# Kernel optimization log

Hardware: AMD Instinct MI355X
Metric: run time of the kernel (lower is better)

The kernel has to match this reference:

```python
import jax, jax.numpy as jnp
import numpy as np

L = 262144
C = 64           # in_channels == out_channels (required by zeros_like scatter)
NUM_MODES = 64

def setup_inputs() -> dict:
    key = jax.random.key(0)
    k1, k2, k3, k4 = jax.random.split(key, 4)
    u = jax.random.normal(k1, (L, C), dtype=jnp.float32)
    y = jax.random.uniform(k2, (1, 1), dtype=jnp.float32)
    scale = 1.0 / (C * C)
    K = scale * jax.random.normal(k3, (2, C, C, NUM_MODES), dtype=jnp.float32)
    # glorot_normal for square (C, C)
    W = jax.random.normal(k4, (C, C), dtype=jnp.float32) * jnp.sqrt(2.0 / (C + C))
    return {"u": u, "y": y, "K": K, "W": W}

def reference(u, y, K, W):
    num_modes = K.shape[-1]
    out_ch = W.shape[0]
    # conditioner: spectral (global) branch
    u_hat = jnp.fft.rfft(u, axis=0)                      # (L//2+1, C) complex64
    Kc = K[0] + 1j * K[1]                                # (C, C, num_modes)
    z_modes = jnp.einsum('xi,iox->xo', u_hat[:num_modes], Kc)  # (num_modes, C)
    z_global = jnp.zeros_like(u_hat).at[:num_modes, :].set(z_modes)
    # conditioner: local branch (gather one spatial row, apply W)
    length = u.shape[0]
    idx = jnp.int32(y * length)[0][0]
    z_local = jnp.dot(W, u[idx, :out_ch])                # (C,)
    # basefield: inverse transform + local shift
    n = 2 * (z_global.shape[0] - 1)                      # == L
    s = jnp.fft.irfft(z_global, n=n, axis=0)             # (L, C)
    return s + z_local
```

## Files before the change

### kernel.cpp

```cpp
#include <hip/hip_runtime.h>

#define LN 262144
#define LMASK 262143
#define NCH 64
#define NBF 512
#define INV_L (1.0f/262144.0f)
#define BSTR 38
#define ISTR 138
#define XSTR 66

typedef short short8 __attribute__((ext_vector_type(8)));
typedef float f32x4 __attribute__((ext_vector_type(4)));

union s8i4 { int4 i; short8 s; };

static __device__ __forceinline__ unsigned pkbf(float lo, float hi) {
    union { float f; unsigned u; } a, b; a.f = lo; b.f = hi;
    return __builtin_amdgcn_perm(b.u, a.u, 0x07060302u);
}
static __device__ __forceinline__ short8 pk8(const float* v) {
    s8i4 cv;
    cv.i = make_int4(pkbf(v[0], v[1]), pkbf(v[2], v[3]),
                     pkbf(v[4], v[5]), pkbf(v[6], v[7]));
    return cv.s;
}
static __device__ __forceinline__ unsigned short f2bf_t(float x) {
    union { float f; unsigned u; } v; v.f = x;
    return (unsigned short)(v.u >> 16);
}
static __device__ __forceinline__ float bf2f(unsigned short b) {
    union { unsigned u; float f; } v; v.u = ((unsigned)b) << 16;
    return v.f;
}
static __device__ __forceinline__ float fsin01(float rev) {
    float r; asm("v_sin_f32 %0, %1" : "=v"(r) : "v"(rev)); return r;
}
static __device__ __forceinline__ float fcos01(float rev) {
    float r; asm("v_cos_f32 %0, %1" : "=v"(r) : "v"(rev)); return r;
}

__global__ __launch_bounds__(256, 2) void fno_fwd(const float* __restrict__ u,
                                                  unsigned* __restrict__ part_w) {
    __shared__ __align__(16) unsigned short Bt[4][64 * BSTR];
    const int tid = threadIdx.x;
    const int lane = tid & 63;
    const int w = tid >> 6;
    const int l15 = lane & 15;
    const int hk = lane >> 4;
    const int kkst = tid >> 3;
    const int gst = tid & 7;
    const int n0 = blockIdx.x * 512;
    const int m = w * 16 + l15;

    float cR[8], nsR[8];
    #pragma unroll
    for (int j = 0; j < 8; ++j) {
        int ph = (m * (n0 + hk * 8 + j)) & LMASK;
        cR[j] = fcos01((float)ph * INV_L);
        nsR[j] = -fsin01((float)ph * INV_L);
    }
    float cD, sD;
    {
        int ph = (m * 32) & LMASK;
        cD = fcos01((float)ph * INV_L);
        sD = fsin01((float)ph * INV_L);
    }

    f32x4 accC[4], accS[4];
    #pragma unroll
    for (int t = 0; t < 4; ++t) { accC[t] = (f32x4){0,0,0,0}; accS[t] = (f32x4){0,0,0,0}; }

    const float* __restrict__ ub = u + (size_t)(n0 + kkst) * NCH + gst * 8;
    const size_t sub = 32 * NCH;
    const size_t sup = 64 * NCH;

#define STAGE(BUF, VA, VB) do {                                            \
        float uv_[8] = {(VA).x, (VA).y, (VA).z, (VA).w,                    \
                        (VB).x, (VB).y, (VB).z, (VB).w};                   \
        _Pragma("unroll")                                                  \
        for (int q_ = 0; q_ < 8; ++q_)                                     \
            Bt[BUF][(gst * 8 + q_) * BSTR + kkst] = f2bf_t(uv_[q_]);       \
    } while (0)

    float4 r0a = *(const float4*)(ub);
    float4 r0b = *(const float4*)(ub + 4);
    float4 r1a = *(const float4*)(ub + sub);
    float4 r1b = *(const float4*)(ub + sub + 4);
    STAGE(0, r0a, r0b);
    STAGE(1, r1a, r1b);
    r0a = *(const float4*)(ub + sup);
    r0b = *(const float4*)(ub + sup + 4);
    r1a = *(const float4*)(ub + sup + sub);
    r1b = *(const float4*)(ub + sup + sub + 4);

    for (int ss = 0; ss < 8; ++ss) {
        __syncthreads();
        const int cp = ss & 1;
        if (ss + 1 < 8) {
            STAGE((cp ^ 1) * 2 + 0, r0a, r0b);
            STAGE((cp ^ 1) * 2 + 1, r1a, r1b);
        }
        if (ss + 2 < 8) {
            const float* pn = ub + (size_t)(ss + 2) * sup;
            r0a = *(const float4*)(pn);
            r0b = *(const float4*)(pn + 4);
            r1a = *(const float4*)(pn + sub);
            r1b = *(const float4*)(pn + sub + 4);
        }
        #pragma unroll
        for (int st = 0; st < 2; ++st) {
            const short8 aC = pk8(cR);
            const short8 aS = pk8(nsR);
            #pragma unroll
            for (int j = 0; j < 8; ++j) {
                float c2 = cR[j] * cD + nsR[j] * sD;
                nsR[j] = nsR[j] * cD - cR[j] * sD;
                cR[j] = c2;
            }
            const unsigned short* bt = Bt[cp * 2 + st];
            #pragma unroll
            for (int tn = 0; tn < 4; ++tn) {
                const short8 bf = *(const short8*)&bt[(tn * 16 + l15) * BSTR + hk * 8];
                accC[tn] = __builtin_amdgcn_mfma_f32_16x16x32_bf16(aC, bf, accC[tn], 0, 0, 0);
                accS[tn] = __builtin_amdgcn_mfma_f32_16x16x32_bf16(aS, bf, accS[tn], 0, 0, 0);
            }
        }
    }
#undef STAGE
    unsigned* basew = part_w + (size_t)blockIdx.x * 4096;
    #pragma unroll
    for (int tn = 0; tn < 4; ++tn) {
        #pragma unroll
        for (int r = 0; r < 4; ++r) {
            int k = w * 16 + hk * 4 + r;
            int i = tn * 16 + l15;
            basew[k * 64 + i] = pkbf(accC[tn][r], accS[tn][r]);
        }
    }
}

__global__ __launch_bounds__(256) void fno_red(const unsigned* __restrict__ part_w,
                                               float* __restrict__ uhat) {
    __shared__ float redR[16][17], redI[16][17];
    const int tid = threadIdx.x;
    const int c = tid & 15;
    const int h = tid >> 4;
    const int j0 = blockIdx.x * 16;

    float aR = 0.f, aI = 0.f;
    #pragma unroll 8
    for (int b = h; b < NBF; b += 16) {
        unsigned v = part_w[(size_t)b * 4096 + j0 + c];
        aR += bf2f((unsigned short)(v & 0xffff));
        aI += bf2f((unsigned short)(v >> 16));
    }
    redR[h][c] = aR;
    redI[h][c] = aI;
    __syncthreads();
    if (tid < 32) {
        const int cc = tid & 15;
        float s = 0.f;
        if (tid < 16) {
            #pragma unroll
            for (int hh = 0; hh < 16; ++hh) s += redR[hh][cc];
            uhat[j0 + cc] = s;
        } else {
            #pragma unroll
            for (int hh = 0; hh < 16; ++hh) s += redI[hh][cc];
            uhat[4096 + j0 + cc] = s;
        }
    }
}

__global__ __launch_bounds__(256) void fno_coef(const float* __restrict__ uhat,
                                                const float* __restrict__ Kt,
                                                const float* __restrict__ W,
                                                const float* __restrict__ u,
                                                const float* __restrict__ y,
                                                float* __restrict__ coef) {
    __shared__ float sm[640];
    const int tid = threadIdx.x;
    const int o = tid & 63;
    const int q = tid >> 6;
    if (blockIdx.x == 64) {
        float* zl4 = sm;
        const int idx = (int)(y[0] * (float)LN);
        float zl = 0.f;
        #pragma unroll 4
        for (int ii = q * 16; ii < q * 16 + 16; ++ii)
            zl = fmaf(W[o * 64 + ii], u[(size_t)idx * 64 + ii], zl);
        zl4[q * 64 + o] = zl;
        __syncthreads();
        if (tid < 64)
            coef[8192 + tid] = zl4[tid] + zl4[64 + tid] + zl4[128 + tid] + zl4[192 + tid];
        return;
    }
    const int k = blockIdx.x;
    float* uh = sm;
    float* zr4 = sm + 128;
    float* zi4 = zr4 + 256;
    if (tid < 128) uh[tid] = uhat[(tid >> 6) * 4096 + k * 64 + (tid & 63)];
    __syncthreads();
    float zr = 0.f, zi = 0.f;
    #pragma unroll 4
    for (int ii = q * 16; ii < q * 16 + 16; ++ii) {
        float k0v = Kt[(size_t)(ii * 64 + o) * 64 + k];
        float k1v = Kt[262144 + (size_t)(ii * 64 + o) * 64 + k];
        zr = fmaf(uh[ii], k0v, fmaf(-uh[64 + ii], k1v, zr));
        zi = fmaf(uh[ii], k1v, fmaf(uh[64 + ii], k0v, zi));
    }
    zr4[q * 64 + o] = zr;
    zi4[q * 64 + o] = zi;
    __syncthreads();
    if (tid < 64) {
        float zrs = zr4[tid] + zr4[64 + tid] + zr4[128 + tid] + zr4[192 + tid];
        float zis = zi4[tid] + zi4[64 + tid] + zi4[128 + tid] + zi4[192 + tid];
        if (k == 0) {
            coef[tid] = zrs * INV_L;
            coef[4096 + tid] = 0.f;
        } else {
            coef[k * 64 + tid] = 2.f * zrs * INV_L;
            coef[4096 + k * 64 + tid] = -2.f * zis * INV_L;
        }
    }
}

__global__ __launch_bounds__(256, 3) void fno_inv(const float* __restrict__ coef,
                                                  float* __restrict__ out) {
    __shared__ __align__(16) char ismem[17920];
    unsigned short* Bs = (unsigned short*)ismem;
    float* zloc = (float*)(ismem + 17664);
    const int tid = threadIdx.x;
    const int lane = tid & 63;
    const int w = tid >> 6;
    const int l15 = lane & 15;
    const int hk = lane >> 4;

    for (int e = tid; e < 4096; e += 256) {
        int mm = e >> 6, ch = e & 63;
        Bs[ch * ISTR + mm] = f2bf_t(coef[e]);
        Bs[ch * ISTR + 64 + mm] = f2bf_t(coef[4096 + e]);
    }
    if (tid < 64) zloc[tid] = coef[8192 + tid];
    __syncthreads();

    const int rl = lane >> 4;
    const int cq = lane & 15;
    float4 zv = *(const float4*)&zloc[cq * 4];

    short8 bfr[4][4];
    #pragma unroll
    for (int ks = 0; ks < 4; ++ks)
        #pragma unroll
        for (int tn = 0; tn < 4; ++tn)
            bfr[ks][tn] = *(const short8*)&Bs[(tn * 16 + l15) * ISTR + ks * 32 + hk * 8];
    __syncthreads();

    float* xpw = (float*)ismem + w * 16 * XSTR;

    for (int p = 0; p < 4; ++p) {
        const int nbase = blockIdx.x * 256 + (p * 4 + w) * 16;
        const int row = nbase + l15;
        float cstp = fcos01((float)row * INV_L);
        float sstp = fsin01((float)row * INV_L);

        short8 aF[4];
        #pragma unroll
        for (int h = 0; h < 2; ++h) {
            const int m0 = h * 32 + hk * 8;
            const int ph = (row * m0) & LMASK;
            float c = fcos01((float)ph * INV_L);
            float s = fsin01((float)ph * INV_L);
            float cv[8], sv[8];
            #pragma unroll
            for (int jj = 0; jj < 8; ++jj) {
                cv[jj] = c; sv[jj] = s;
                float c2 = c * cstp - s * sstp;
                s = fmaf(s, cstp, c * sstp);
                c = c2;
            }
            aF[h] = pk8(cv);
            aF[2 + h] = pk8(sv);
        }

        f32x4 acc[4];
        #pragma unroll
        for (int tn = 0; tn < 4; ++tn) acc[tn] = (f32x4){0,0,0,0};
        #pragma unroll
        for (int ks = 0; ks < 4; ++ks)
            #pragma unroll
            for (int tn = 0; tn < 4; ++tn)
                acc[tn] = __builtin_amdgcn_mfma_f32_16x16x32_bf16(aF[ks], bfr[ks][tn], acc[tn], 0, 0, 0);

        #pragma unroll
        for (int tn = 0; tn < 4; ++tn)
            #pragma unroll
            for (int r = 0; r < 4; ++r)
                xpw[(hk * 4 + r) * XSTR + tn * 16 + l15] = acc[tn][r];
        asm volatile("s_waitcnt lgkmcnt(0)" ::: "memory");
        #pragma unroll
        for (int rg = 0; rg < 4; ++rg) {
            const int rowl = rg * 4 + rl;
            float4 v = *(const float4*)&xpw[rowl * XSTR + cq * 4];
            v.x += zv.x; v.y += zv.y; v.z += zv.z; v.w += zv.w;
            *(float4*)(out + (size_t)(nbase + rowl) * NCH + cq * 4) = v;
        }
        asm volatile("s_waitcnt lgkmcnt(0)" ::: "memory");
    }
}

extern "C" void kernel_launch(void* const* d_in, const int* in_sizes, int n_in,
                              void* d_out, int out_size, void* d_ws, size_t ws_size,
                              hipStream_t stream) {
    const float* u = (const float*)d_in[0];
    const float* y = (const float*)d_in[1];
    const float* K = (const float*)d_in[2];
    const float* W = (const float*)d_in[3];
    float* out = (float*)d_out;

    unsigned* part_w = (unsigned*)d_ws;
    float* uhat = (float*)((char*)d_ws + 8388608);
    float* coef = uhat + 8192;

    fno_fwd<<<NBF, 256, 0, stream>>>(u, part_w);
    fno_red<<<256, 256, 0, stream>>>(part_w, uhat);
    fno_coef<<<65, 256, 0, stream>>>(uhat, K, W, u, y, coef);
    fno_inv<<<1024, 256, 0, stream>>>(coef, out);
}
```

Before: 63.93 us.

## Transpose inverse MFMA to store outputs directly and simplify forward staging

```diff
diff --git a/kernel.cpp b/kernel.cpp
--- a/kernel.cpp
+++ b/kernel.cpp
@@ -7,7 +7,6 @@
 #define INV_L (1.0f/262144.0f)
 #define BSTR 38
 #define ISTR 138
-#define XSTR 66
 
 typedef short short8 __attribute__((ext_vector_type(8)));
 typedef float f32x4 __attribute__((ext_vector_type(4)));
@@ -41,7 +40,7 @@
 
 __global__ __launch_bounds__(256, 2) void fno_fwd(const float* __restrict__ u,
                                                   unsigned* __restrict__ part_w) {
-    __shared__ __align__(16) unsigned short Bt[4][64 * BSTR];
+    __shared__ __align__(16) unsigned short Bt[2][64 * BSTR];
     const int tid = threadIdx.x;
     const int lane = tid & 63;
     const int w = tid >> 6;
@@ -50,6 +49,7 @@
     const int kkst = tid >> 3;
     const int gst = tid & 7;
     const int n0 = blockIdx.x * 512;
+    const int ksteps = 16;
     const int m = w * 16 + l15;
 
     float cR[8], nsR[8];
@@ -71,8 +71,7 @@
     for (int t = 0; t < 4; ++t) { accC[t] = (f32x4){0,0,0,0}; accS[t] = (f32x4){0,0,0,0}; }
 
     const float* __restrict__ ub = u + (size_t)(n0 + kkst) * NCH + gst * 8;
-    const size_t sub = 32 * NCH;
-    const size_t sup = 64 * NCH;
+    const size_t tstep = 32 * NCH;
 
 #define STAGE(BUF, VA, VB) do {                                            \
         float uv_[8] = {(VA).x, (VA).y, (VA).z, (VA).w,                    \
@@ -82,48 +81,39 @@
             Bt[BUF][(gst * 8 + q_) * BSTR + kkst] = f2bf_t(uv_[q_]);       \
     } while (0)
 
-    float4 r0a = *(const float4*)(ub);
-    float4 r0b = *(const float4*)(ub + 4);
-    float4 r1a = *(const float4*)(ub + sub);
-    float4 r1b = *(const float4*)(ub + sub + 4);
-    STAGE(0, r0a, r0b);
-    STAGE(1, r1a, r1b);
-    r0a = *(const float4*)(ub + sup);
-    r0b = *(const float4*)(ub + sup + 4);
-    r1a = *(const float4*)(ub + sup + sub);
-    r1b = *(const float4*)(ub + sup + sub + 4);
-
-    for (int ss = 0; ss < 8; ++ss) {
+    float4 a0 = *(const float4*)(ub);
+    float4 a1 = *(const float4*)(ub + 4);
+    float4 b0 = *(const float4*)(ub + tstep);
+    float4 b1 = *(const float4*)(ub + tstep + 4);
+    STAGE(0, a0, a1);
+    a0 = b0; a1 = b1;
+    b0 = *(const float4*)(ub + 2 * tstep);
+    b1 = *(const float4*)(ub + 2 * tstep + 4);
+
+    for (int t = 0; t < ksteps; ++t) {
         __syncthreads();
-        const int cp = ss & 1;
-        if (ss + 1 < 8) {
-            STAGE((cp ^ 1) * 2 + 0, r0a, r0b);
-            STAGE((cp ^ 1) * 2 + 1, r1a, r1b);
-        }
-        if (ss + 2 < 8) {
-            const float* pn = ub + (size_t)(ss + 2) * sup;
-            r0a = *(const float4*)(pn);
-            r0b = *(const float4*)(pn + 4);
-            r1a = *(const float4*)(pn + sub);
-            r1b = *(const float4*)(pn + sub + 4);
-        }
-        #pragma unroll
-        for (int st = 0; st < 2; ++st) {
-            const short8 aC = pk8(cR);
-            const short8 aS = pk8(nsR);
-            #pragma unroll
-            for (int j = 0; j < 8; ++j) {
-                float c2 = cR[j] * cD + nsR[j] * sD;
-                nsR[j] = nsR[j] * cD - cR[j] * sD;
-                cR[j] = c2;
-            }
-            const unsigned short* bt = Bt[cp * 2 + st];
-            #pragma unroll
-            for (int tn = 0; tn < 4; ++tn) {
-                const short8 bf = *(const short8*)&bt[(tn * 16 + l15) * BSTR + hk * 8];
-                accC[tn] = __builtin_amdgcn_mfma_f32_16x16x32_bf16(aC, bf, accC[tn], 0, 0, 0);
-                accS[tn] = __builtin_amdgcn_mfma_f32_16x16x32_bf16(aS, bf, accS[tn], 0, 0, 0);
-            }
+        if (t + 1 < ksteps)
+            STAGE((t + 1) & 1, a0, a1);
+        a0 = b0; a1 = b1;
+        if (t + 3 < ksteps) {
+            const float* pn = ub + (size_t)(t + 3) * tstep;
+            b0 = *(const float4*)(pn);
+            b1 = *(const float4*)(pn + 4);
+        }
+        const short8 aC = pk8(cR);
+        const short8 aS = pk8(nsR);
+        #pragma unroll
+        for (int j = 0; j < 8; ++j) {
+            float c2 = cR[j] * cD + nsR[j] * sD;
+            nsR[j] = nsR[j] * cD - cR[j] * sD;
+            cR[j] = c2;
+        }
+        const unsigned short* bt = Bt[t & 1];
+        #pragma unroll
+        for (int tn = 0; tn < 4; ++tn) {
+            const short8 bf = *(const short8*)&bt[(tn * 16 + l15) * BSTR + hk * 8];
+            accC[tn] = __builtin_amdgcn_mfma_f32_16x16x32_bf16(aC, bf, accC[tn], 0, 0, 0);
+            accS[tn] = __builtin_amdgcn_mfma_f32_16x16x32_bf16(aS, bf, accS[tn], 0, 0, 0);
         }
     }
 #undef STAGE
@@ -227,9 +217,8 @@
 
 __global__ __launch_bounds__(256, 3) void fno_inv(const float* __restrict__ coef,
                                                   float* __restrict__ out) {
-    __shared__ __align__(16) char ismem[17920];
-    unsigned short* Bs = (unsigned short*)ismem;
-    float* zloc = (float*)(ismem + 17664);
+    __shared__ __align__(16) unsigned short Bs[64 * ISTR];
+    __shared__ float zloc[64];
     const int tid = threadIdx.x;
     const int lane = tid & 63;
     const int w = tid >> 6;
@@ -244,19 +233,16 @@
     if (tid < 64) zloc[tid] = coef[8192 + tid];
     __syncthreads();
 
-    const int rl = lane >> 4;
-    const int cq = lane & 15;
-    float4 zv = *(const float4*)&zloc[cq * 4];
-
-    short8 bfr[4][4];
+    short8 afr[4][4];
     #pragma unroll
     for (int ks = 0; ks < 4; ++ks)
         #pragma unroll
         for (int tn = 0; tn < 4; ++tn)
-            bfr[ks][tn] = *(const short8*)&Bs[(tn * 16 + l15) * ISTR + ks * 32 + hk * 8];
-    __syncthreads();
-
-    float* xpw = (float*)ismem + w * 16 * XSTR;
+            afr[ks][tn] = *(const short8*)&Bs[(tn * 16 + l15) * ISTR + ks * 32 + hk * 8];
+    float4 zv[4];
+    #pragma unroll
+    for (int tn = 0; tn < 4; ++tn)
+        zv[tn] = *(const float4*)&zloc[tn * 16 + hk * 4];
 
     for (int p = 0; p < 4; ++p) {
         const int nbase = blockIdx.x * 256 + (p * 4 + w) * 16;
@@ -264,7 +250,7 @@
         float cstp = fcos01((float)row * INV_L);
         float sstp = fsin01((float)row * INV_L);
 
-        short8 aF[4];
+        short8 bF[4];
         #pragma unroll
         for (int h = 0; h < 2; ++h) {
             const int m0 = h * 32 + hk * 8;
@@ -279,8 +265,8 @@
                 s = fmaf(s, cstp, c * sstp);
                 c = c2;
             }
-            aF[h] = pk8(cv);
-            aF[2 + h] = pk8(sv);
+            bF[h] = pk8(cv);
+            bF[2 + h] = pk8(sv);
         }
 
         f32x4 acc[4];
@@ -290,22 +276,15 @@
         for (int ks = 0; ks < 4; ++ks)
             #pragma unroll
             for (int tn = 0; tn < 4; ++tn)
-                acc[tn] = __builtin_amdgcn_mfma_f32_16x16x32_bf16(aF[ks], bfr[ks][tn], acc[tn], 0, 0, 0);
-
-        #pragma unroll
-        for (int tn = 0; tn < 4; ++tn)
-            #pragma unroll
-            for (int r = 0; r < 4; ++r)
-                xpw[(hk * 4 + r) * XSTR + tn * 16 + l15] = acc[tn][r];
-        asm volatile("s_waitcnt lgkmcnt(0)" ::: "memory");
-        #pragma unroll
-        for (int rg = 0; rg < 4; ++rg) {
-            const int rowl = rg * 4 + rl;
-            float4 v = *(const float4*)&xpw[rowl * XSTR + cq * 4];
-            v.x += zv.x; v.y += zv.y; v.z += zv.z; v.w += zv.w;
-            *(float4*)(out + (size_t)(nbase + rowl) * NCH + cq * 4) = v;
-        }
-        asm volatile("s_waitcnt lgkmcnt(0)" ::: "memory");
+                acc[tn] = __builtin_amdgcn_mfma_f32_16x16x32_bf16(afr[ks][tn], bF[ks], acc[tn], 0, 0, 0);
+
+        float* po = out + (size_t)row * NCH;
+        #pragma unroll
+        for (int tn = 0; tn < 4; ++tn) {
+            float4 v = make_float4(acc[tn][0] + zv[tn].x, acc[tn][1] + zv[tn].y,
+                                   acc[tn][2] + zv[tn].z, acc[tn][3] + zv[tn].w);
+            *(float4*)(po + tn * 16 + hk * 4) = v;
+        }
     }
 }
 
```

Result: slower. 80.33 us (+25.7%).
